# Optimization experiments

Measured on AMD Instinct MI355X. Metric: run time of the kernel, lower is better.

## Reference

```python
import jax, jax.numpy as jnp
import numpy as np

DIM = 1024
NUM_HEADS = 16
HEAD_DIM = DIM // NUM_HEADS


def setup_inputs() -> dict:
    key = jax.random.key(0)
    k1, k2, k3 = jax.random.split(key, 3)
    x = jax.random.normal(k1, (4, 1024, DIM), dtype=jnp.float32)
    # match nn.Linear init scale roughly: small weights
    Wqkv = jax.random.normal(k2, (3 * DIM, DIM), dtype=jnp.float32) * (1.0 / np.sqrt(DIM))
    Wproj = jax.random.normal(k3, (DIM, DIM), dtype=jnp.float32) * (1.0 / np.sqrt(DIM))
    bproj = jnp.zeros((DIM,), dtype=jnp.float32)
    return {"x": x, "Wqkv": Wqkv, "Wproj": Wproj, "bproj": bproj}


def reference(x, Wqkv, Wproj, bproj):
    bsz, tsz, chans = x.shape
    # fused QKV projection (qkv_bias=False): [B,T,3C]
    qkv = jnp.einsum("btc,oc->bto", x, Wqkv)
    qkv = qkv.reshape(bsz, tsz, 3, NUM_HEADS, HEAD_DIM)
    q = qkv[:, :, 0].transpose(0, 2, 1, 3)  # [B,H,T,D]
    k = qkv[:, :, 1].transpose(0, 2, 1, 3)
    v = qkv[:, :, 2].transpose(0, 2, 1, 3)
    scale = 1.0 / np.sqrt(HEAD_DIM)
    logits = jnp.einsum("bhqd,bhkd->bhqk", q, k) * scale  # [B,H,T,T]
    attn = jax.nn.softmax(logits, axis=-1)
    out = jnp.einsum("bhqk,bhkd->bhqd", attn, v)  # [B,H,T,D]
    out = out.transpose(0, 2, 1, 3).reshape(bsz, tsz, chans)
    return jnp.einsum("btc,oc->bto", out, Wproj) + bproj
```

## Files before the change

### kernel.cpp

```cpp
#include <hip/hip_runtime.h>
#include <hip/hip_bf16.h>

typedef __attribute__((ext_vector_type(8))) short bfrag8;
typedef __attribute__((ext_vector_type(4))) short bfrag4;
typedef __attribute__((ext_vector_type(4))) float floatx4;

typedef unsigned short ushort_t;
typedef unsigned int uint_t;

static __device__ __forceinline__ uint_t pk_bf16(float a, float b) {
    union { __hip_bfloat162 h; uint_t u; } cv;
    cv.h = __float22bfloat162_rn(make_float2(a, b));
    return cv.u;
}

static __device__ __forceinline__ void gl_lds16(const ushort_t* g, ushort_t* l) {
    __builtin_amdgcn_global_load_lds(
        (const __attribute__((address_space(1))) void*)g,
        (__attribute__((address_space(3))) void*)l, 16, 0, 0);
}

__global__ __launch_bounds__(256)
void cvt_all(const float* __restrict__ x, const float* __restrict__ wqkv,
             const float* __restrict__ wproj, ushort_t* __restrict__ xb,
             ushort_t* __restrict__ wqkvb, ushort_t* __restrict__ wprojb) {
    int blk = blockIdx.x;
    const float* src; ushort_t* dst; int base;
    if (blk < 4096)      { src = x;     dst = xb;     base = blk; }
    else if (blk < 7168) { src = wqkv;  dst = wqkvb;  base = blk - 4096; }
    else                 { src = wproj; dst = wprojb; base = blk - 7168; }
    int i = (base * 256 + threadIdx.x) * 4;
    float4 f = *(const float4*)(src + i);
    uint_t lo = pk_bf16(f.x, f.y);
    uint_t hi = pk_bf16(f.z, f.w);
    uint2 u = {lo, hi};
    *(uint2*)(dst + i) = u;
}

__global__ __launch_bounds__(256, 2)
void qkv_gemm(const ushort_t* __restrict__ A, const ushort_t* __restrict__ B,
              ushort_t* __restrict__ qp, ushort_t* __restrict__ kp,
              ushort_t* __restrict__ vp) {
    const int K = 1024;
    __shared__ ushort_t As[128 * 64];
    __shared__ ushort_t Bs[128 * 64];
    int tid = threadIdx.x;
    int wave = __builtin_amdgcn_readfirstlane(tid >> 6);
    int lane = tid & 63;
    int quad = lane >> 4, l16 = lane & 15;
    int wm = (wave >> 1) * 64, wn = (wave & 1) * 64;
    int m0 = blockIdx.y * 128, n0 = blockIdx.x * 128;

    int rl = lane >> 3;
    int gc = (lane & 7) ^ rl;

    floatx4 acc[4][4] = {};

    const ushort_t* Ag = A + (size_t)m0 * K;
    const ushort_t* Bg = B + (size_t)n0 * K;

    for (int k0 = 0; k0 < K; k0 += 64) {
        __syncthreads();
#pragma unroll
        for (int i = 0; i < 4; i++) {
            int row = wave * 32 + i * 8 + rl;
            gl_lds16(Ag + (size_t)row * K + k0 + gc * 8, &As[(wave * 32 + i * 8) * 64]);
            gl_lds16(Bg + (size_t)row * K + k0 + gc * 8, &Bs[(wave * 32 + i * 8) * 64]);
        }
        __syncthreads();
#pragma unroll
        for (int ks = 0; ks < 2; ks++) {
            bfrag8 af[4], bf[4];
#pragma unroll
            for (int mt = 0; mt < 4; mt++) {
                int r = wm + mt * 16 + l16;
                af[mt] = *(const bfrag8*)&As[r * 64 + ((4 * ks + quad) ^ (r & 7)) * 8];
            }
#pragma unroll
            for (int nt = 0; nt < 4; nt++) {
                int r = wn + nt * 16 + l16;
                bf[nt] = *(const bfrag8*)&Bs[r * 64 + ((4 * ks + quad) ^ (r & 7)) * 8];
            }
#pragma unroll
            for (int mt = 0; mt < 4; mt++)
#pragma unroll
                for (int nt = 0; nt < 4; nt++)
                    acc[mt][nt] = __builtin_amdgcn_mfma_f32_16x16x32_bf16(
                        af[mt], bf[nt], acc[mt][nt], 0, 0, 0);
        }
    }

#pragma unroll
    for (int mt = 0; mt < 4; mt++) {
#pragma unroll
        for (int nt = 0; nt < 4; nt++) {
            int o = n0 + wn + nt * 16 + l16;
            int s = o >> 10;
            int rem = o & 1023;
            int h = rem >> 6, d = rem & 63;
            ushort_t* dst = (s == 0) ? qp : (s == 1) ? kp : vp;
            float scl = (s == 0) ? 0.125f : 1.0f;
            uint_t p01 = pk_bf16(acc[mt][nt][0] * scl, acc[mt][nt][1] * scl);
            uint_t p23 = pk_bf16(acc[mt][nt][2] * scl, acc[mt][nt][3] * scl);
            ushort_t pv[4] = {(ushort_t)p01, (ushort_t)(p01 >> 16),
                              (ushort_t)p23, (ushort_t)(p23 >> 16)};
#pragma unroll
            for (int r = 0; r < 4; r++) {
                int t = m0 + wm + mt * 16 + quad * 4 + r;
                int b = t >> 10, tt = t & 1023;
                dst[((size_t)(b * 16 + h) * 1024 + tt) * 64 + d] = pv[r];
            }
        }
    }
}

__global__ __launch_bounds__(256)
void transpose_v(const ushort_t* __restrict__ v, ushort_t* __restrict__ vT) {
    int bh = blockIdx.y;
    int t0 = blockIdx.x * 64;
    __shared__ ushort_t tile[64][72];
    int tid = threadIdx.x;
    int r = tid >> 3;
    int c = (tid & 7) * 8;
#pragma unroll
    for (int i = 0; i < 2; i++) {
        int t = r + i * 32;
        *(uint4*)&tile[t][c] = *(const uint4*)&v[((size_t)bh * 1024 + t0 + t) * 64 + c];
    }
    __syncthreads();
#pragma unroll
    for (int i = 0; i < 2; i++) {
        int d = r + i * 32;
        union { ushort_t u[8]; uint4 v4; } tmp;
#pragma unroll
        for (int j = 0; j < 8; j++) tmp.u[j] = tile[c + j][d];
        *(uint4*)&vT[((size_t)bh * 64 + d) * 1024 + t0 + c] = tmp.v4;
    }
}

__global__ __launch_bounds__(256, 2)
void attn_kernel(const ushort_t* __restrict__ q, const ushort_t* __restrict__ k,
                 const ushort_t* __restrict__ vT, ushort_t* __restrict__ out) {
    int id = blockIdx.x;
    int bh = (id & 7) + ((id >> 6) << 3);
    int qt = (id >> 3) & 7;
    const ushort_t* qb = q + (size_t)bh * 1024 * 64;
    const ushort_t* kb = k + (size_t)bh * 1024 * 64;
    const ushort_t* vtb = vT + (size_t)bh * 64 * 1024;
    int tid = threadIdx.x;
    int wave = __builtin_amdgcn_readfirstlane(tid >> 6);
    int lane = tid & 63;
    int quad = lane >> 4, l16 = lane & 15;
    int q0 = qt * 128 + wave * 32;

    __shared__ ushort_t Ks[64 * 64];
    __shared__ ushort_t VTs[64 * 64];
    __shared__ ushort_t Ps[4][32][68];

    int rl = lane >> 3;
    int gc = (lane & 7) ^ rl;

    bfrag8 qf[2][2];
#pragma unroll
    for (int mt = 0; mt < 2; mt++)
#pragma unroll
        for (int ks = 0; ks < 2; ks++)
            qf[mt][ks] = *(const bfrag8*)&qb[(size_t)(q0 + mt * 16 + l16) * 64 + ks * 32 + quad * 8];

    floatx4 oacc[2][4] = {};
    float li[2][4] = {};

    for (int kt = 0; kt < 16; kt++) {
        __syncthreads();
#pragma unroll
        for (int i = 0; i < 2; i++) {
            int row = wave * 16 + i * 8 + rl;
            gl_lds16(kb + (size_t)(kt * 64 + row) * 64 + gc * 8, &Ks[(wave * 16 + i * 8) * 64]);
            gl_lds16(vtb + (size_t)row * 1024 + kt * 64 + gc * 8, &VTs[(wave * 16 + i * 8) * 64]);
        }
        __syncthreads();

        floatx4 s[2][4] = {};
#pragma unroll
        for (int ks = 0; ks < 2; ks++) {
            bfrag8 bfg[4];
#pragma unroll
            for (int nt = 0; nt < 4; nt++) {
                int r = nt * 16 + l16;
                bfg[nt] = *(const bfrag8*)&Ks[r * 64 + ((4 * ks + quad) ^ (r & 7)) * 8];
            }
#pragma unroll
            for (int mt = 0; mt < 2; mt++)
#pragma unroll
                for (int nt = 0; nt < 4; nt++)
                    s[mt][nt] = __builtin_amdgcn_mfma_f32_16x16x32_bf16(
                        qf[mt][ks], bfg[nt], s[mt][nt], 0, 0, 0);
        }

#pragma unroll
        for (int mt = 0; mt < 2; mt++)
#pragma unroll
            for (int r = 0; r < 4; r++) {
                float p0 = __expf(s[mt][0][r]);
                float p1 = __expf(s[mt][1][r]);
                float p2 = __expf(s[mt][2][r]);
                float p3 = __expf(s[mt][3][r]);
                uint_t c01 = pk_bf16(p0, p1);
                uint_t c23 = pk_bf16(p2, p3);
                int prow = mt * 16 + quad * 4 + r;
                Ps[wave][prow][0 + l16]  = (ushort_t)c01;
                Ps[wave][prow][16 + l16] = (ushort_t)(c01 >> 16);
                Ps[wave][prow][32 + l16] = (ushort_t)c23;
                Ps[wave][prow][48 + l16] = (ushort_t)(c23 >> 16);
                li[mt][r] += (p0 + p1) + (p2 + p3);
            }

#pragma unroll
        for (int ks = 0; ks < 2; ks++) {
            bfrag8 pa[2], vbf[4];
#pragma unroll
            for (int mt = 0; mt < 2; mt++) {
                const ushort_t* pp = &Ps[wave][mt * 16 + l16][ks * 32 + quad * 8];
                bfrag4 plo = *(const bfrag4*)pp;
                bfrag4 phi = *(const bfrag4*)(pp + 4);
                pa[mt] = __builtin_shufflevector(plo, phi, 0, 1, 2, 3, 4, 5, 6, 7);
            }
#pragma unroll
            for (int nd = 0; nd < 4; nd++) {
                int r = nd * 16 + l16;
                vbf[nd] = *(const bfrag8*)&VTs[r * 64 + ((4 * ks + quad) ^ (r & 7)) * 8];
            }
#pragma unroll
            for (int mt = 0; mt < 2; mt++)
#pragma unroll
                for (int nd = 0; nd < 4; nd++)
                    oacc[mt][nd] = __builtin_amdgcn_mfma_f32_16x16x32_bf16(
                        pa[mt], vbf[nd], oacc[mt][nd], 0, 0, 0);
        }
    }

    int b = bh >> 4, h = bh & 15;
#pragma unroll
    for (int mt = 0; mt < 2; mt++) {
        float inv[4];
#pragma unroll
        for (int r = 0; r < 4; r++) {
            float s0 = li[mt][r];
            s0 += __shfl_xor(s0, 1);
            s0 += __shfl_xor(s0, 2);
            s0 += __shfl_xor(s0, 4);
            s0 += __shfl_xor(s0, 8);
            inv[r] = 1.0f / s0;
        }
#pragma unroll
        for (int nd = 0; nd < 4; nd++) {
            uint_t c01 = pk_bf16(oacc[mt][nd][0] * inv[0], oacc[mt][nd][1] * inv[1]);
            uint_t c23 = pk_bf16(oacc[mt][nd][2] * inv[2], oacc[mt][nd][3] * inv[3]);
            ushort_t pv[4] = {(ushort_t)c01, (ushort_t)(c01 >> 16),
                              (ushort_t)c23, (ushort_t)(c23 >> 16)};
#pragma unroll
            for (int r = 0; r < 4; r++) {
                int t = q0 + mt * 16 + quad * 4 + r;
                int c = h * 64 + nd * 16 + l16;
                out[((size_t)(b * 1024 + t)) * 1024 + c] = pv[r];
            }
        }
    }
}

__global__ __launch_bounds__(256, 2)
void proj_gemm(const ushort_t* __restrict__ A, const ushort_t* __restrict__ B,
               const float* __restrict__ bias, float* __restrict__ out) {
    const int K = 1024;
    __shared__ ushort_t As[64 * 64];
    __shared__ ushort_t Bs[128 * 64];
    int tid = threadIdx.x;
    int wave = __builtin_amdgcn_readfirstlane(tid >> 6);
    int lane = tid & 63;
    int quad = lane >> 4, l16 = lane & 15;
    int wm = (wave >> 1) * 32, wn = (wave & 1) * 64;
    int m0 = blockIdx.y * 64, n0 = blockIdx.x * 128;

    int rl = lane >> 3;
    int gc = (lane & 7) ^ rl;

    floatx4 acc[2][4] = {};

    const ushort_t* Ag = A + (size_t)m0 * K;
    const ushort_t* Bg = B + (size_t)n0 * K;

    for (int k0 = 0; k0 < K; k0 += 64) {
        __syncthreads();
#pragma unroll
        for (int i = 0; i < 2; i++) {
            int row = wave * 16 + i * 8 + rl;
            gl_lds16(Ag + (size_t)row * K + k0 + gc * 8, &As[(wave * 16 + i * 8) * 64]);
        }
#pragma unroll
        for (int i = 0; i < 4; i++) {
            int row = wave * 32 + i * 8 + rl;
            gl_lds16(Bg + (size_t)row * K + k0 + gc * 8, &Bs[(wave * 32 + i * 8) * 64]);
        }
        __syncthreads();
#pragma unroll
        for (int ks = 0; ks < 2; ks++) {
            bfrag8 af[2], bf[4];
#pragma unroll
            for (int mt = 0; mt < 2; mt++) {
                int r = wm + mt * 16 + l16;
                af[mt] = *(const bfrag8*)&As[r * 64 + ((4 * ks + quad) ^ (r & 7)) * 8];
            }
#pragma unroll
            for (int nt = 0; nt < 4; nt++) {
                int r = wn + nt * 16 + l16;
                bf[nt] = *(const bfrag8*)&Bs[r * 64 + ((4 * ks + quad) ^ (r & 7)) * 8];
            }
#pragma unroll
            for (int mt = 0; mt < 2; mt++)
#pragma unroll
                for (int nt = 0; nt < 4; nt++)
                    acc[mt][nt] = __builtin_amdgcn_mfma_f32_16x16x32_bf16(
                        af[mt], bf[nt], acc[mt][nt], 0, 0, 0);
        }
    }

#pragma unroll
    for (int mt = 0; mt < 2; mt++) {
#pragma unroll
        for (int nt = 0; nt < 4; nt++) {
            int o = n0 + wn + nt * 16 + l16;
            float bv = bias[o];
#pragma unroll
            for (int r = 0; r < 4; r++) {
                int t = m0 + wm + mt * 16 + quad * 4 + r;
                out[(size_t)t * 1024 + o] = acc[mt][nt][r] + bv;
            }
        }
    }
}

extern "C" void kernel_launch(void* const* d_in, const int* in_sizes, int n_in,
                              void* d_out, int out_size, void* d_ws, size_t ws_size,
                              hipStream_t stream) {
    const float* x     = (const float*)d_in[0];
    const float* Wqkv  = (const float*)d_in[1];
    const float* Wproj = (const float*)d_in[2];
    const float* bproj = (const float*)d_in[3];
    float* out = (float*)d_out;

    char* ws = (char*)d_ws;
    ushort_t* xb     = (ushort_t*)(ws);
    ushort_t* wqkvb  = (ushort_t*)(ws + ((size_t)8 << 20));
    ushort_t* wprojb = (ushort_t*)(ws + ((size_t)14 << 20));
    ushort_t* qp     = (ushort_t*)(ws + ((size_t)16 << 20));
    ushort_t* kp     = (ushort_t*)(ws + ((size_t)24 << 20));
    ushort_t* vp     = (ushort_t*)(ws + ((size_t)32 << 20));
    ushort_t* vTp    = (ushort_t*)(ws + ((size_t)40 << 20));
    ushort_t* attn   = (ushort_t*)(ws + ((size_t)48 << 20));

    cvt_all<<<8192, 256, 0, stream>>>(x, Wqkv, Wproj, xb, wqkvb, wprojb);
    qkv_gemm<<<dim3(24, 32), 256, 0, stream>>>(xb, wqkvb, qp, kp, vp);
    transpose_v<<<dim3(16, 64), 256, 0, stream>>>(vp, vTp);
    attn_kernel<<<512, 256, 0, stream>>>(qp, kp, vTp, attn);
    proj_gemm<<<dim3(8, 64), 256, 0, stream>>>(attn, wprojb, bproj, out);
}
```

Baseline: 166.2 us.

## Compute transposed scores to keep P in registers and enlarge key tiles

Result: no change. 169.1 us (+1.7%).

```diff
diff --git a/kernel.cpp b/kernel.cpp
--- a/kernel.cpp
+++ b/kernel.cpp
@@ -13,6 +13,22 @@
     cv.h = __float22bfloat162_rn(make_float2(a, b));
     return cv.u;
 }
+
+#if __has_builtin(__builtin_amdgcn_mfma_f32_16x16x16_bf16)
+static __device__ __forceinline__ floatx4 mfma16(bfrag4 a, bfrag4 b, floatx4 c) {
+    return __builtin_amdgcn_mfma_f32_16x16x16_bf16(a, b, c, 0, 0, 0);
+}
+#elif __has_builtin(__builtin_amdgcn_mfma_f32_16x16x16bf16_1k)
+static __device__ __forceinline__ floatx4 mfma16(bfrag4 a, bfrag4 b, floatx4 c) {
+    return __builtin_amdgcn_mfma_f32_16x16x16bf16_1k(a, b, c, 0, 0, 0);
+}
+#else
+static __device__ __forceinline__ floatx4 mfma16(bfrag4 a, bfrag4 b, floatx4 c) {
+    bfrag8 az = {a[0], 0, a[1], 0, a[2], 0, a[3], 0};
+    bfrag8 bz = {b[0], 0, b[1], 0, b[2], 0, b[3], 0};
+    return __builtin_amdgcn_mfma_f32_16x16x32_bf16(az, bz, c, 0, 0, 0);
+}
+#endif
 
 static __device__ __forceinline__ void gl_lds16(const ushort_t* g, ushort_t* l) {
     __builtin_amdgcn_global_load_lds(
@@ -153,9 +169,8 @@
     int quad = lane >> 4, l16 = lane & 15;
     int q0 = qt * 128 + wave * 32;
 
-    __shared__ ushort_t Ks[64 * 64];
-    __shared__ ushort_t VTs[64 * 64];
-    __shared__ ushort_t Ps[4][32][68];
+    __shared__ ushort_t Ks[128 * 64];
+    __shared__ ushort_t VTs[64 * 136];
 
     int rl = lane >> 3;
     int gc = (lane & 7) ^ rl;
@@ -168,94 +183,96 @@
             qf[mt][ks] = *(const bfrag8*)&qb[(size_t)(q0 + mt * 16 + l16) * 64 + ks * 32 + quad * 8];
 
     floatx4 oacc[2][4] = {};
-    float li[2][4] = {};
-
-    for (int kt = 0; kt < 16; kt++) {
-        __syncthreads();
-#pragma unroll
-        for (int i = 0; i < 2; i++) {
-            int row = wave * 16 + i * 8 + rl;
-            gl_lds16(kb + (size_t)(kt * 64 + row) * 64 + gc * 8, &Ks[(wave * 16 + i * 8) * 64]);
-            gl_lds16(vtb + (size_t)row * 1024 + kt * 64 + gc * 8, &VTs[(wave * 16 + i * 8) * 64]);
-        }
-        __syncthreads();
-
-        floatx4 s[2][4] = {};
-#pragma unroll
-        for (int ks = 0; ks < 2; ks++) {
-            bfrag8 bfg[4];
-#pragma unroll
-            for (int nt = 0; nt < 4; nt++) {
-                int r = nt * 16 + l16;
-                bfg[nt] = *(const bfrag8*)&Ks[r * 64 + ((4 * ks + quad) ^ (r & 7)) * 8];
-            }
+    float li[2] = {0.f, 0.f};
+
+    int vd = tid >> 2;
+    int vc = tid & 3;
+
+    for (int kt = 0; kt < 8; kt++) {
+        uint4 vv[4];
+#pragma unroll
+        for (int i = 0; i < 4; i++)
+            vv[i] = *(const uint4*)&vtb[(size_t)vd * 1024 + kt * 128 + (vc + i * 4) * 8];
+        __syncthreads();
+#pragma unroll
+        for (int i = 0; i < 4; i++) {
+            int row = wave * 32 + i * 8 + rl;
+            gl_lds16(kb + (size_t)(kt * 128 + row) * 64 + gc * 8, &Ks[(wave * 32 + i * 8) * 64]);
+        }
+#pragma unroll
+        for (int i = 0; i < 4; i++)
+            *(uint4*)&VTs[vd * 136 + (vc + i * 4) * 8] = vv[i];
+        __syncthreads();
+
+#pragma unroll
+        for (int half = 0; half < 2; half++) {
+            floatx4 st[2][4] = {};
+#pragma unroll
+            for (int ks = 0; ks < 2; ks++) {
+                bfrag8 kf[4];
+#pragma unroll
+                for (int tt = 0; tt < 4; tt++) {
+                    int r = (half * 4 + tt) * 16 + l16;
+                    kf[tt] = *(const bfrag8*)&Ks[r * 64 + ((4 * ks + quad) ^ (r & 7)) * 8];
+                }
+#pragma unroll
+                for (int mt = 0; mt < 2; mt++)
+#pragma unroll
+                    for (int tt = 0; tt < 4; tt++)
+                        st[mt][tt] = __builtin_amdgcn_mfma_f32_16x16x32_bf16(
+                            kf[tt], qf[mt][ks], st[mt][tt], 0, 0, 0);
+            }
+
+            bfrag4 pf[2][4];
 #pragma unroll
             for (int mt = 0; mt < 2; mt++)
 #pragma unroll
-                for (int nt = 0; nt < 4; nt++)
-                    s[mt][nt] = __builtin_amdgcn_mfma_f32_16x16x32_bf16(
-                        qf[mt][ks], bfg[nt], s[mt][nt], 0, 0, 0);
-        }
-
-#pragma unroll
-        for (int mt = 0; mt < 2; mt++)
-#pragma unroll
-            for (int r = 0; r < 4; r++) {
-                float p0 = __expf(s[mt][0][r]);
-                float p1 = __expf(s[mt][1][r]);
-                float p2 = __expf(s[mt][2][r]);
-                float p3 = __expf(s[mt][3][r]);
-                uint_t c01 = pk_bf16(p0, p1);
-                uint_t c23 = pk_bf16(p2, p3);
-                int prow = mt * 16 + quad * 4 + r;
-                Ps[wave][prow][0 + l16]  = (ushort_t)c01;
-                Ps[wave][prow][16 + l16] = (ushort_t)(c01 >> 16);
-                Ps[wave][prow][32 + l16] = (ushort_t)c23;
-                Ps[wave][prow][48 + l16] = (ushort_t)(c23 >> 16);
-                li[mt][r] += (p0 + p1) + (p2 + p3);
-            }
-
-#pragma unroll
-        for (int ks = 0; ks < 2; ks++) {
-            bfrag8 pa[2], vbf[4];
-#pragma unroll
-            for (int mt = 0; mt < 2; mt++) {
-                const ushort_t* pp = &Ps[wave][mt * 16 + l16][ks * 32 + quad * 8];
-                bfrag4 plo = *(const bfrag4*)pp;
-                bfrag4 phi = *(const bfrag4*)(pp + 4);
-                pa[mt] = __builtin_shufflevector(plo, phi, 0, 1, 2, 3, 4, 5, 6, 7);
-            }
-#pragma unroll
-            for (int nd = 0; nd < 4; nd++) {
-                int r = nd * 16 + l16;
-                vbf[nd] = *(const bfrag8*)&VTs[r * 64 + ((4 * ks + quad) ^ (r & 7)) * 8];
-            }
-#pragma unroll
-            for (int mt = 0; mt < 2; mt++)
+                for (int tt = 0; tt < 4; tt++) {
+                    float p0 = __expf(st[mt][tt][0]);
+                    float p1 = __expf(st[mt][tt][1]);
+                    float p2 = __expf(st[mt][tt][2]);
+                    float p3 = __expf(st[mt][tt][3]);
+                    li[mt] += (p0 + p1) + (p2 + p3);
+                    union { uint2 u; bfrag4 f; } pk;
+                    pk.u.x = pk_bf16(p0, p1);
+                    pk.u.y = pk_bf16(p2, p3);
+                    pf[mt][tt] = pk.f;
+                }
+
+#pragma unroll
+            for (int tt = 0; tt < 4; tt++) {
+                int keyoff = (half * 4 + tt) * 16;
+                bfrag4 vb[4];
 #pragma unroll
                 for (int nd = 0; nd < 4; nd++)
-                    oacc[mt][nd] = __builtin_amdgcn_mfma_f32_16x16x32_bf16(
-                        pa[mt], vbf[nd], oacc[mt][nd], 0, 0, 0);
-        }
+                    vb[nd] = *(const bfrag4*)&VTs[(nd * 16 + l16) * 136 + keyoff + quad * 4];
+#pragma unroll
+                for (int mt = 0; mt < 2; mt++)
+#pragma unroll
+                    for (int nd = 0; nd < 4; nd++)
+                        oacc[mt][nd] = mfma16(pf[mt][tt], vb[nd], oacc[mt][nd]);
+            }
+        }
+    }
+
+    float inv[2][4];
+#pragma unroll
+    for (int mt = 0; mt < 2; mt++) {
+        float s0 = li[mt];
+        s0 += __shfl_xor(s0, 16);
+        s0 += __shfl_xor(s0, 32);
+#pragma unroll
+        for (int r = 0; r < 4; r++)
+            inv[mt][r] = 1.0f / __shfl(s0, quad * 4 + r);
     }
 
     int b = bh >> 4, h = bh & 15;
 #pragma unroll
-    for (int mt = 0; mt < 2; mt++) {
-        float inv[4];
-#pragma unroll
-        for (int r = 0; r < 4; r++) {
-            float s0 = li[mt][r];
-            s0 += __shfl_xor(s0, 1);
-            s0 += __shfl_xor(s0, 2);
-            s0 += __shfl_xor(s0, 4);
-            s0 += __shfl_xor(s0, 8);
-            inv[r] = 1.0f / s0;
-        }
+    for (int mt = 0; mt < 2; mt++)
 #pragma unroll
         for (int nd = 0; nd < 4; nd++) {
-            uint_t c01 = pk_bf16(oacc[mt][nd][0] * inv[0], oacc[mt][nd][1] * inv[1]);
-            uint_t c23 = pk_bf16(oacc[mt][nd][2] * inv[2], oacc[mt][nd][3] * inv[3]);
+            uint_t c01 = pk_bf16(oacc[mt][nd][0] * inv[mt][0], oacc[mt][nd][1] * inv[mt][1]);
+            uint_t c23 = pk_bf16(oacc[mt][nd][2] * inv[mt][2], oacc[mt][nd][3] * inv[mt][3]);
             ushort_t pv[4] = {(ushort_t)c01, (ushort_t)(c01 >> 16),
                               (ushort_t)c23, (ushort_t)(c23 >> 16)};
 #pragma unroll
@@ -265,7 +282,6 @@
                 out[((size_t)(b * 1024 + t)) * 1024 + c] = pv[r];
             }
         }
-    }
 }
 
 __global__ __launch_bounds__(256, 2)
```
